# Performance work log

Hardware: AMD Instinct MI355X
Metric: run time of the kernel (lower is better)

## Reference

```python
import jax, jax.numpy as jnp
import numpy as np

EPS = 1e-5  # BatchNorm eps

def _bn(x):
    # BatchNorm1d(affine=False) in training mode: per-agent, per-feature batch stats
    m = jnp.mean(x, axis=1, keepdims=True)
    v = jnp.var(x, axis=1, keepdims=True)
    return (x - m) / jnp.sqrt(v + EPS)

def _lrelu(x):
    return jax.nn.leaky_relu(x, 0.01)

def setup_inputs() -> dict:
    key = jax.random.key(0)
    ks = jax.random.split(key, 14)
    A, B, IN, OUT, H, K = 8, 32768, 128, 32, 128, 4
    D = H // K
    s = 0.05
    return {
        "states": jax.random.normal(ks[0], (A, B, IN), jnp.float32),
        "actions": jax.random.normal(ks[1], (A, B, OUT), jnp.float32),
        "enc_w": jax.random.normal(ks[2], (A, IN + OUT, H), jnp.float32) * s,
        "enc_b": jax.random.normal(ks[3], (A, H), jnp.float32) * s,
        "aenc_w": jax.random.normal(ks[4], (A, OUT, H), jnp.float32) * s,
        "aenc_b": jax.random.normal(ks[5], (A, H), jnp.float32) * s,
        "key_w": jax.random.normal(ks[6], (K, H, D), jnp.float32) * s,
        "sel_w": jax.random.normal(ks[7], (K, H, D), jnp.float32) * s,
        "val_w": jax.random.normal(ks[8], (K, H, D), jnp.float32) * s,
        "val_b": jax.random.normal(ks[9], (K, D), jnp.float32) * s,
        "c1_w": jax.random.normal(ks[10], (A, 2 * H, H), jnp.float32) * s,
        "c1_b": jax.random.normal(ks[11], (A, H), jnp.float32) * s,
        "c2_w": jax.random.normal(ks[12], (A, H, 1), jnp.float32) * s,
        "c2_b": jax.random.normal(ks[13], (A, 1), jnp.float32) * s,
    }

def reference(states, actions, enc_w, enc_b, aenc_w, aenc_b,
              key_w, sel_w, val_w, val_b, c1_w, c1_b, c2_w, c2_b):
    A, B, _ = states.shape
    # per-agent state-action encodings: [A,B,H]
    sa = _bn(jnp.concatenate([states, actions], axis=-1))
    sa_enc = _lrelu(jnp.einsum('abi,aih->abh', sa, enc_w) + enc_b[:, None, :])
    # per-agent action encodings: [A,B,H]
    a_in = _bn(actions)
    a_enc = _lrelu(jnp.einsum('abi,aih->abh', a_in, aenc_w) + aenc_b[:, None, :])
    # per-head keys/values/selectors: [K,A,B,D]
    keys = jnp.einsum('abh,khd->kabd', a_enc, key_w)
    vals = _lrelu(jnp.einsum('abh,khd->kabd', a_enc, val_w) + val_b[:, None, None, :])
    sels = jnp.einsum('abh,khd->kabd', sa_enc, sel_w)
    D = keys.shape[-1]
    # attention logits over other agents: [K,B,A_query,A_key], self excluded
    logits = jnp.einsum('kibd,kjbd->kbij', sels, keys) / jnp.sqrt(jnp.float32(D))
    self_mask = jnp.eye(A, dtype=bool)[None, None]
    probs = jax.nn.softmax(jnp.where(self_mask, -jnp.inf, logits), axis=-1)
    # attended values: [K,A,B,D] -> concat heads -> [A,B,K*D]
    other = jnp.einsum('kbij,kjbd->kibd', probs, vals)
    other_cat = jnp.transpose(other, (1, 2, 0, 3)).reshape(A, B, -1)
    # per-agent critics on [sa_enc, attended]: [A,B,1]
    critic_in = jnp.concatenate([sa_enc, other_cat], axis=-1)
    h = _lrelu(jnp.einsum('abi,aih->abh', critic_in, c1_w) + c1_b[:, None, :])
    q = jnp.einsum('abh,aho->abo', h, c2_w) + c2_b[:, None, :]
    return q
```

## Files before the change

kernel.cpp:

```cpp
#include <hip/hip_runtime.h>
#include <hip/hip_bf16.h>
#include <stdint.h>

#define A_N 8
#define B_N 32768
#define IN_N 128
#define OUT_N 32
#define SAF 160
#define H_N 128
#define D_N 32
#define KD_N 128
#define CIN_N 256
#define CHUNKS 128
#define EPSV 1e-5f
#define ENC_KP 192

typedef unsigned int u32;
typedef unsigned short u16;
typedef __attribute__((ext_vector_type(8))) short short8;
typedef __attribute__((ext_vector_type(4))) float floatx4;

__device__ __forceinline__ float bf_lo(u32 u){ return __uint_as_float(u << 16); }
__device__ __forceinline__ float bf_hi(u32 u){ return __uint_as_float(u & 0xffff0000u); }
__device__ __forceinline__ float bf2f(u16 b){ return __uint_as_float(((u32)b) << 16); }
__device__ __forceinline__ u16 f2bf(float f){
  u32 u = __float_as_uint(f);
  return (u16)((u + 0x7fffu + ((u >> 16) & 1u)) >> 16);
}
__device__ __forceinline__ float lrelu(float x){ return x > 0.f ? x : 0.01f * x; }

__global__ __launch_bounds__(256) void k_stats(
    const float* __restrict__ states, const float* __restrict__ actions,
    float* __restrict__ part)
{
  int a = blockIdx.y;
  int chunk = blockIdx.x;
  int t = threadIdx.x;
  int r0 = chunk * (B_N / CHUNKS);
  __shared__ float red[512];
  {
    int f = t & 127, half = t >> 7;
    const float* p = states + ((size_t)a * B_N + r0 + half) * IN_N + f;
    float s1 = 0.f, s2 = 0.f;
    for (int it = 0; it < 128; ++it){
      float v = p[(size_t)(2 * it) * IN_N];
      s1 += v; s2 += v * v;
    }
    red[t] = s1; red[256 + t] = s2;
    __syncthreads();
    if (t < 128){
      float a1 = red[t] + red[t + 128];
      float a2 = red[256 + t] + red[256 + t + 128];
      size_t o = (((size_t)a * CHUNKS + chunk) * SAF + t) * 2;
      part[o] = a1; part[o + 1] = a2;
    }
    __syncthreads();
  }
  {
    int f = t & 31, g = t >> 5;
    const float* p = actions + ((size_t)a * B_N + r0 + g) * OUT_N + f;
    float s1 = 0.f, s2 = 0.f;
    for (int it = 0; it < 32; ++it){
      float v = p[(size_t)(8 * it) * OUT_N];
      s1 += v; s2 += v * v;
    }
    red[t] = s1; red[256 + t] = s2;
    __syncthreads();
    if (t < 32){
      float a1 = 0.f, a2 = 0.f;
      #pragma unroll
      for (int gg = 0; gg < 8; ++gg){
        a1 += red[t + 32 * gg];
        a2 += red[256 + t + 32 * gg];
      }
      size_t o = (((size_t)a * CHUNKS + chunk) * SAF + 128 + t) * 2;
      part[o] = a1; part[o + 1] = a2;
    }
  }
}

__global__ void k_finalize(const float* __restrict__ part,
                           float* __restrict__ meanArr, float* __restrict__ istdArr)
{
  int idx = blockIdx.x * blockDim.x + threadIdx.x;
  if (idx >= A_N * SAF) return;
  int a = idx / SAF, f = idx % SAF;
  float s1 = 0.f, s2 = 0.f;
  for (int c = 0; c < CHUNKS; ++c){
    size_t o = (((size_t)a * CHUNKS + c) * SAF + f) * 2;
    s1 += part[o]; s2 += part[o + 1];
  }
  float m = s1 * (1.f / B_N);
  float v = s2 * (1.f / B_N) - m * m;
  if (v < 0.f) v = 0.f;
  meanArr[idx] = m;
  istdArr[idx] = rsqrtf(v + EPSV);
}

__device__ __forceinline__ void packpair(float w, u16* __restrict__ dh,
                                         u16* __restrict__ dl, int i){
  u16 h = f2bf(w);
  dh[i] = h;
  dl[i] = f2bf(w - bf2f(h));
}

__global__ __launch_bounds__(256) void k_pack(
    const float* __restrict__ enc_w, const float* __restrict__ aenc_w,
    const float* __restrict__ key_w, const float* __restrict__ sel_w,
    const float* __restrict__ val_w, const float* __restrict__ c1_w,
    u16* __restrict__ encH, u16* __restrict__ encL,
    u16* __restrict__ aencH, u16* __restrict__ aencL,
    u16* __restrict__ keyH, u16* __restrict__ selH, u16* __restrict__ valH,
    u16* __restrict__ c1H, u16* __restrict__ c1L)
{
  int i = blockIdx.x * 256 + threadIdx.x;
  const int S0 = A_N * H_N * ENC_KP;
  const int S1 = A_N * H_N * OUT_N;
  const int S2 = KD_N * H_N;
  const int S5 = A_N * H_N * CIN_N;
  if (i < S0){
    int a = i / (H_N * ENC_KP); int r = i % (H_N * ENC_KP);
    int n = r / ENC_KP; int k = r % ENC_KP;
    float v = (k < SAF) ? enc_w[((size_t)a * SAF + k) * H_N + n] : 0.f;
    packpair(v, encH, encL, i);
    return;
  }
  i -= S0;
  if (i < S1){
    int a = i / (H_N * OUT_N); int r = i % (H_N * OUT_N);
    int n = r / OUT_N; int k = r % OUT_N;
    packpair(aenc_w[((size_t)a * OUT_N + k) * H_N + n], aencH, aencL, i);
    return;
  }
  i -= S1;
  if (i < 3 * S2){
    int which = i / S2; int j = i % S2;
    int n = j / H_N, k = j % H_N;
    const float* w = (which == 0) ? key_w : ((which == 1) ? sel_w : val_w);
    u16* dh = (which == 0) ? keyH : ((which == 1) ? selH : valH);
    dh[j] = f2bf(w[(((size_t)(n >> 5)) * H_N + k) * D_N + (n & 31)]);
    return;
  }
  i -= 3 * S2;
  if (i < S5){
    int a = i / (H_N * CIN_N); int r = i % (H_N * CIN_N);
    int n = r / CIN_N; int k = r % CIN_N;
    packpair(c1_w[((size_t)a * CIN_N + k) * H_N + n], c1H, c1L, i);
  }
}
#define PACK_TOTAL (A_N*H_N*ENC_KP + A_N*H_N*OUT_N + 3*KD_N*H_N + A_N*H_N*CIN_N)

__global__ __launch_bounds__(256, 3) void k_enc_sel(
    const float* __restrict__ states, const float* __restrict__ actions,
    const float* __restrict__ mean, const float* __restrict__ istd,
    const u16* __restrict__ encH, const u16* __restrict__ encL,
    const float* __restrict__ enc_b,
    const u16* __restrict__ selH,
    u16* __restrict__ sa_enc, u16* __restrict__ sels)
{
  int a = blockIdx.y; int row0 = blockIdx.x * 128; int t = threadIdx.x;
  int lane = t & 63, wave = t >> 6, l16 = lane & 15, quad = lane >> 4;
  __shared__ __align__(16) u16 S[22528];
  __shared__ __align__(16) float sc[192], sh[192];
  u16* Wh = S;
  u16* Wl = S + 5120;
  u16* Xh = S + 10240;
  u16* Xl = S + 15360;
  u16* T  = S;
  u16* Ws = S + 17408;

  if (t < 192){
    float m = 0.f, s = 0.f;
    if (t < SAF){ m = mean[a * SAF + t]; s = istd[a * SAF + t]; }
    sc[t] = s; sh[t] = -m * s;
  }
  floatx4 acc[2][8];
  #pragma unroll
  for (int mt = 0; mt < 2; ++mt)
    #pragma unroll
    for (int nt = 0; nt < 8; ++nt) acc[mt][nt] = (floatx4){0.f,0.f,0.f,0.f};
  const u16* wbh = encH + (size_t)a * H_N * ENC_KP;
  const u16* wbl = encL + (size_t)a * H_N * ENC_KP;
  __syncthreads();

  for (int k0 = 0; k0 < ENC_KP; k0 += 32){
    for (int c = t; c < 512; c += 256){
      int n = c >> 2, off = (c & 3) * 8;
      *(uint4*)&Wh[n * 40 + off] = *(const uint4*)(wbh + (size_t)n * ENC_KP + k0 + off);
      *(uint4*)&Wl[n * 40 + off] = *(const uint4*)(wbl + (size_t)n * ENC_KP + k0 + off);
    }
    for (int c = t; c < 1024; c += 256){
      int r = c >> 3, kc = (c & 7) * 4, f = k0 + kc;
      size_t row = (size_t)a * B_N + row0 + r;
      float4 v = {0.f, 0.f, 0.f, 0.f};
      if (f < IN_N)     v = *(const float4*)(states + row * IN_N + f);
      else if (f < SAF) v = *(const float4*)(actions + row * OUT_N + (f - IN_N));
      float4 scv = *(const float4*)&sc[f];
      float4 shv = *(const float4*)&sh[f];
      float x0 = fmaf(v.x, scv.x, shv.x), x1 = fmaf(v.y, scv.y, shv.y);
      float x2 = fmaf(v.z, scv.z, shv.z), x3 = fmaf(v.w, scv.w, shv.w);
      u16 h0 = f2bf(x0), h1 = f2bf(x1), h2 = f2bf(x2), h3 = f2bf(x3);
      *(u32*)&Xh[r * 40 + kc]     = (u32)h0 | ((u32)h1 << 16);
      *(u32*)&Xh[r * 40 + kc + 2] = (u32)h2 | ((u32)h3 << 16);
      u16 l0 = f2bf(x0 - bf2f(h0)), l1 = f2bf(x1 - bf2f(h1));
      u16 l2 = f2bf(x2 - bf2f(h2)), l3 = f2bf(x3 - bf2f(h3));
      *(u32*)&Xl[r * 40 + kc]     = (u32)l0 | ((u32)l1 << 16);
      *(u32*)&Xl[r * 40 + kc + 2] = (u32)l2 | ((u32)l3 << 16);
    }
    __syncthreads();
    {
      short8 ah[2], al[2], bh[8], bl[8];
      #pragma unroll
      for (int mt = 0; mt < 2; ++mt){
        int rr = (wave * 32 + mt * 16 + l16) * 40 + quad * 8;
        ah[mt] = *(const short8*)&Xh[rr];
        al[mt] = *(const short8*)&Xl[rr];
      }
      #pragma unroll
      for (int nt = 0; nt < 8; ++nt){
        int rr = (nt * 16 + l16) * 40 + quad * 8;
        bh[nt] = *(const short8*)&Wh[rr];
        bl[nt] = *(const short8*)&Wl[rr];
      }
      #pragma unroll
      for (int mt = 0; mt < 2; ++mt)
        #pragma unroll
        for (int nt = 0; nt < 8; ++nt){
          acc[mt][nt] = __builtin_amdgcn_mfma_f32_16x16x32_bf16(ah[mt], bh[nt], acc[mt][nt], 0,0,0);
          acc[mt][nt] = __builtin_amdgcn_mfma_f32_16x16x32_bf16(ah[mt], bl[nt], acc[mt][nt], 0,0,0);
          acc[mt][nt] = __builtin_amdgcn_mfma_f32_16x16x32_bf16(al[mt], bh[nt], acc[mt][nt], 0,0,0);
        }
    }
    __syncthreads();
  }

  {
    float bv[8];
    #pragma unroll
    for (int nt = 0; nt < 8; ++nt) bv[nt] = enc_b[a * H_N + nt * 16 + l16];
    #pragma unroll
    for (int mt = 0; mt < 2; ++mt)
      #pragma unroll
      for (int nt = 0; nt < 8; ++nt)
        #pragma unroll
        for (int r = 0; r < 4; ++r){
          int rl = wave * 32 + mt * 16 + quad * 4 + r;
          T[rl * 136 + nt * 16 + l16] = f2bf(lrelu(acc[mt][nt][r] + bv[nt]));
        }
  }
  __syncthreads();
  for (int c = t; c < 2048; c += 256){
    int row = c >> 4, col8 = (c & 15) * 8;
    *(uint4*)(sa_enc + ((size_t)a * B_N + row0 + row) * H_N + col8) =
        *(const uint4*)&T[row * 136 + col8];
  }

  #pragma unroll
  for (int mt = 0; mt < 2; ++mt)
    #pragma unroll
    for (int nt = 0; nt < 8; ++nt) acc[mt][nt] = (floatx4){0.f,0.f,0.f,0.f};
  for (int k0 = 0; k0 < H_N; k0 += 32){
    for (int c = t; c < 512; c += 256){
      int n = c >> 2, off = (c & 3) * 8;
      *(uint4*)&Ws[n * 40 + off] = *(const uint4*)(selH + (size_t)n * H_N + k0 + off);
    }
    __syncthreads();
    {
      short8 ah[2], bh[8];
      #pragma unroll
      for (int mt = 0; mt < 2; ++mt)
        ah[mt] = *(const short8*)&T[(wave * 32 + mt * 16 + l16) * 136 + k0 + quad * 8];
      #pragma unroll
      for (int nt = 0; nt < 8; ++nt)
        bh[nt] = *(const short8*)&Ws[(nt * 16 + l16) * 40 + quad * 8];
      #pragma unroll
      for (int mt = 0; mt < 2; ++mt)
        #pragma unroll
        for (int nt = 0; nt < 8; ++nt)
          acc[mt][nt] = __builtin_amdgcn_mfma_f32_16x16x32_bf16(ah[mt], bh[nt], acc[mt][nt], 0,0,0);
    }
    __syncthreads();
  }
  #pragma unroll
  for (int mt = 0; mt < 2; ++mt)
    #pragma unroll
    for (int nt = 0; nt < 8; ++nt)
      #pragma unroll
      for (int r = 0; r < 4; ++r){
        int rl = wave * 32 + mt * 16 + quad * 4 + r;
        T[rl * 136 + nt * 16 + l16] = f2bf(acc[mt][nt][r]);
      }
  __syncthreads();
  for (int c = t; c < 2048; c += 256){
    int row = c >> 4, col8 = (c & 15) * 8;
    *(uint4*)(sels + ((size_t)a * B_N + row0 + row) * H_N + col8) =
        *(const uint4*)&T[row * 136 + col8];
  }
}

__global__ __launch_bounds__(256, 2) void k_aenc_kv(
    const float* __restrict__ actions,
    const float* __restrict__ mean, const float* __restrict__ istd,
    const u16* __restrict__ aencH, const u16* __restrict__ aencL,
    const float* __restrict__ aenc_b,
    const u16* __restrict__ keyH, const u16* __restrict__ valH,
    const float* __restrict__ val_b,
    u16* __restrict__ keys, u16* __restrict__ vals)
{
  int a = blockIdx.y; int row0 = blockIdx.x * 128; int t = threadIdx.x;
  int lane = t & 63, wave = t >> 6, l16 = lane & 15, quad = lane >> 4;
  __shared__ __align__(16) u16 S[35840];
  __shared__ __align__(16) float sc[32], sh[32];
  u16* T  = S;
  u16* WK = S + 17408;
  u16* WV = S + 26624;
  u16* T2 = S + 17408;

  if (t < 32){
    float m = mean[a * SAF + 128 + t], s = istd[a * SAF + 128 + t];
    sc[t] = s; sh[t] = -m * s;
  }
  floatx4 accK[2][8], accV[2][8];
  #pragma unroll
  for (int mt = 0; mt < 2; ++mt)
    #pragma unroll
    for (int nt = 0; nt < 8; ++nt){
      accK[mt][nt] = (floatx4){0.f,0.f,0.f,0.f};
      accV[mt][nt] = (floatx4){0.f,0.f,0.f,0.f};
    }
  __syncthreads();

  {
    u16* Wh1 = S;  u16* Wl1 = S + 5120;
    u16* Xh = S + 10240; u16* Xl = S + 15360;
    const u16* wbh = aencH + (size_t)a * H_N * OUT_N;
    const u16* wbl = aencL + (size_t)a * H_N * OUT_N;
    for (int c = t; c < 512; c += 256){
      int n = c >> 2, off = (c & 3) * 8;
      *(uint4*)&Wh1[n * 40 + off] = *(const uint4*)(wbh + (size_t)n * OUT_N + off);
      *(uint4*)&Wl1[n * 40 + off] = *(const uint4*)(wbl + (size_t)n * OUT_N + off);
    }
    for (int c = t; c < 1024; c += 256){
      int r = c >> 3, kc = (c & 7) * 4;
      size_t row = (size_t)a * B_N + row0 + r;
      float4 v = *(const float4*)(actions + row * OUT_N + kc);
      float4 scv = *(const float4*)&sc[kc];
      float4 shv = *(const float4*)&sh[kc];
      float x0 = fmaf(v.x, scv.x, shv.x), x1 = fmaf(v.y, scv.y, shv.y);
      float x2 = fmaf(v.z, scv.z, shv.z), x3 = fmaf(v.w, scv.w, shv.w);
      u16 h0 = f2bf(x0), h1 = f2bf(x1), h2 = f2bf(x2), h3 = f2bf(x3);
      *(u32*)&Xh[r * 40 + kc]     = (u32)h0 | ((u32)h1 << 16);
      *(u32*)&Xh[r * 40 + kc + 2] = (u32)h2 | ((u32)h3 << 16);
      u16 l0 = f2bf(x0 - bf2f(h0)), l1 = f2bf(x1 - bf2f(h1));
      u16 l2 = f2bf(x2 - bf2f(h2)), l3 = f2bf(x3 - bf2f(h3));
      *(u32*)&Xl[r * 40 + kc]     = (u32)l0 | ((u32)l1 << 16);
      *(u32*)&Xl[r * 40 + kc + 2] = (u32)l2 | ((u32)l3 << 16);
    }
    __syncthreads();
    short8 ah[2], al[2], bh[8], bl[8];
    #pragma unroll
    for (int mt = 0; mt < 2; ++mt){
      int rr = (wave * 32 + mt * 16 + l16) * 40 + quad * 8;
      ah[mt] = *(const short8*)&Xh[rr];
      al[mt] = *(const short8*)&Xl[rr];
    }
    #pragma unroll
    for (int nt = 0; nt < 8; ++nt){
      int rr = (nt * 16 + l16) * 40 + quad * 8;
      bh[nt] = *(const short8*)&Wh1[rr];
      bl[nt] = *(const short8*)&Wl1[rr];
    }
    #pragma unroll
    for (int mt = 0; mt < 2; ++mt)
      #pragma unroll
      for (int nt = 0; nt < 8; ++nt){
        accK[mt][nt] = __builtin_amdgcn_mfma_f32_16x16x32_bf16(ah[mt], bh[nt], accK[mt][nt], 0,0,0);
        accK[mt][nt] = __builtin_amdgcn_mfma_f32_16x16x32_bf16(ah[mt], bl[nt], accK[mt][nt], 0,0,0);
        accK[mt][nt] = __builtin_amdgcn_mfma_f32_16x16x32_bf16(al[mt], bh[nt], accK[mt][nt], 0,0,0);
      }
    __syncthreads();
  }
  {
    float bv[8];
    #pragma unroll
    for (int nt = 0; nt < 8; ++nt) bv[nt] = aenc_b[a * H_N + nt * 16 + l16];
    #pragma unroll
    for (int mt = 0; mt < 2; ++mt)
      #pragma unroll
      for (int nt = 0; nt < 8; ++nt){
        #pragma unroll
        for (int r = 0; r < 4; ++r){
          int rl = wave * 32 + mt * 16 + quad * 4 + r;
          T[rl * 136 + nt * 16 + l16] = f2bf(lrelu(accK[mt][nt][r] + bv[nt]));
        }
        accK[mt][nt] = (floatx4){0.f,0.f,0.f,0.f};
      }
  }

  for (int k0 = 0; k0 < H_N; k0 += 64){
    __syncthreads();
    for (int c = t; c < 1024; c += 256){
      int n = c >> 3, off = (c & 7) * 8;
      *(uint4*)&WK[n * 72 + off] = *(const uint4*)(keyH + (size_t)n * H_N + k0 + off);
      *(uint4*)&WV[n * 72 + off] = *(const uint4*)(valH + (size_t)n * H_N + k0 + off);
    }
    __syncthreads();
    #pragma unroll
    for (int ks = 0; ks < 64; ks += 32){
      short8 ah[2], bk[8], bv[8];
      #pragma unroll
      for (int mt = 0; mt < 2; ++mt)
        ah[mt] = *(const short8*)&T[(wave * 32 + mt * 16 + l16) * 136 + k0 + ks + quad * 8];
      #pragma unroll
      for (int nt = 0; nt < 8; ++nt){
        int rr = (nt * 16 + l16) * 72 + ks + quad * 8;
        bk[nt] = *(const short8*)&WK[rr];
        bv[nt] = *(const short8*)&WV[rr];
      }
      #pragma unroll
      for (int mt = 0; mt < 2; ++mt)
        #pragma unroll
        for (int nt = 0; nt < 8; ++nt){
          accK[mt][nt] = __builtin_amdgcn_mfma_f32_16x16x32_bf16(ah[mt], bk[nt], accK[mt][nt], 0,0,0);
          accV[mt][nt] = __builtin_amdgcn_mfma_f32_16x16x32_bf16(ah[mt], bv[nt], accV[mt][nt], 0,0,0);
        }
    }
  }
  __syncthreads();
  {
    float bv[8];
    #pragma unroll
    for (int nt = 0; nt < 8; ++nt) bv[nt] = val_b[nt * 16 + l16];
    #pragma unroll
    for (int mt = 0; mt < 2; ++mt)
      #pragma unroll
      for (int nt = 0; nt < 8; ++nt)
        #pragma unroll
        for (int r = 0; r < 4; ++r){
          int rl = wave * 32 + mt * 16 + quad * 4 + r;
          T[rl * 136 + nt * 16 + l16]  = f2bf(lrelu(accV[mt][nt][r] + bv[nt]));
          T2[rl * 136 + nt * 16 + l16] = f2bf(accK[mt][nt][r]);
        }
  }
  __syncthreads();
  for (int c = t; c < 2048; c += 256){
    int row = c >> 4, col8 = (c & 15) * 8;
    *(uint4*)(vals + ((size_t)a * B_N + row0 + row) * H_N + col8) =
        *(const uint4*)&T[row * 136 + col8];
    *(uint4*)(keys + ((size_t)a * B_N + row0 + row) * H_N + col8) =
        *(const uint4*)&T2[row * 136 + col8];
  }
}

__global__ __launch_bounds__(256) void k_attn(
    const u16* __restrict__ sels, const u16* __restrict__ keys,
    const u16* __restrict__ vals, u16* __restrict__ other)
{
  int b0 = blockIdx.x * 8;
  int t = threadIdx.x;
  __shared__ __align__(16) u16 sS[8192], sK[8192], sV[8192];
  u32* dS = (u32*)sS; u32* dK = (u32*)sK; u32* dV = (u32*)sV;
  #pragma unroll
  for (int a = 0; a < 8; ++a){
    size_t go = ((size_t)a * B_N + b0) * KD_N;
    const u32* gs = (const u32*)(sels + go);
    const u32* gk = (const u32*)(keys + go);
    const u32* gv = (const u32*)(vals + go);
    dS[a * 512 + t] = gs[t]; dS[a * 512 + 256 + t] = gs[256 + t];
    dK[a * 512 + t] = gk[t]; dK[a * 512 + 256 + t] = gk[256 + t];
    dV[a * 512 + t] = gv[t]; dV[a * 512 + 256 + t] = gv[256 + t];
  }
  __syncthreads();
  int i = t & 7, p = t >> 3;
  int k = p & 3, bl = p >> 2;
  int base_i = (i * 8 + bl) * 128 + k * 32;
  float si[32];
  {
    const u32* S32 = (const u32*)&sS[base_i];
    #pragma unroll
    for (int d2 = 0; d2 < 16; ++d2){
      u32 u = S32[d2];
      si[2 * d2] = bf_lo(u); si[2 * d2 + 1] = bf_hi(u);
    }
  }
  float lg[8];
  #pragma unroll
  for (int j = 0; j < 8; ++j){
    const u32* K32 = (const u32*)&sK[(j * 8 + bl) * 128 + k * 32];
    float acc = 0.f;
    #pragma unroll
    for (int d2 = 0; d2 < 16; ++d2){
      u32 u = K32[d2];
      acc = fmaf(si[2 * d2], bf_lo(u), acc);
      acc = fmaf(si[2 * d2 + 1], bf_hi(u), acc);
    }
    lg[j] = acc * 0.17677669529663689f;
  }
  float mx = -3.0e38f;
  #pragma unroll
  for (int j = 0; j < 8; ++j) if (j != i) mx = fmaxf(mx, lg[j]);
  float pe[8], se = 0.f;
  #pragma unroll
  for (int j = 0; j < 8; ++j){
    pe[j] = (j == i) ? 0.f : __expf(lg[j] - mx);
    se += pe[j];
  }
  float inv = 1.f / se;
  #pragma unroll
  for (int j = 0; j < 8; ++j) pe[j] *= inv;
  __align__(16) u16 ob[32];
  #pragma unroll
  for (int d2 = 0; d2 < 16; ++d2){
    float acc0 = 0.f, acc1 = 0.f;
    #pragma unroll
    for (int j = 0; j < 8; ++j){
      u32 u = *(const u32*)&sV[(j * 8 + bl) * 128 + k * 32 + 2 * d2];
      acc0 = fmaf(pe[j], bf_lo(u), acc0);
      acc1 = fmaf(pe[j], bf_hi(u), acc1);
    }
    ob[2 * d2] = f2bf(acc0); ob[2 * d2 + 1] = f2bf(acc1);
  }
  uint4* dst = (uint4*)(other + ((size_t)i * B_N + (b0 + bl)) * KD_N + k * 32);
  const uint4* s4 = (const uint4*)ob;
  #pragma unroll
  for (int c = 0; c < 4; ++c) dst[c] = s4[c];
}

__global__ __launch_bounds__(256, 3) void k_critic(
    const u16* __restrict__ sa_enc, const u16* __restrict__ other,
    const u16* __restrict__ c1H, const u16* __restrict__ c1L,
    const float* __restrict__ c1_b,
    const float* __restrict__ c2w, const float* __restrict__ c2b,
    float* __restrict__ qout)
{
  int a = blockIdx.y; int row0 = blockIdx.x * 128; int t = threadIdx.x;
  int lane = t & 63, wave = t >> 6, l16 = lane & 15, quad = lane >> 4;
  __shared__ __align__(16) u16 Xs[5120];
  __shared__ __align__(16) u16 Wh[5120];
  __shared__ __align__(16) u16 Wl[5120];
  floatx4 acc[2][8];
  #pragma unroll
  for (int mt = 0; mt < 2; ++mt)
    #pragma unroll
    for (int nt = 0; nt < 8; ++nt) acc[mt][nt] = (floatx4){0.f,0.f,0.f,0.f};
  const u16* wbh = c1H + (size_t)a * H_N * CIN_N;
  const u16* wbl = c1L + (size_t)a * H_N * CIN_N;

  for (int k0 = 0; k0 < CIN_N; k0 += 32){
    for (int c = t; c < 512; c += 256){
      int n = c >> 2, off = (c & 3) * 8;
      *(uint4*)&Wh[n * 40 + off] = *(const uint4*)(wbh + (size_t)n * CIN_N + k0 + off);
      *(uint4*)&Wl[n * 40 + off] = *(const uint4*)(wbl + (size_t)n * CIN_N + k0 + off);
    }
    for (int c = t; c < 512; c += 256){
      int r = c >> 2, off = (c & 3) * 8;
      int fo = k0 + off;
      const u16* src = sa_enc;
      if (fo >= H_N){ src = other; fo -= H_N; }
      *(uint4*)&Xs[r * 40 + off] =
          *(const uint4*)(src + ((size_t)a * B_N + row0 + r) * H_N + fo);
    }
    __syncthreads();
    {
      short8 ah[2], bh[8], bl[8];
      #pragma unroll
      for (int mt = 0; mt < 2; ++mt)
        ah[mt] = *(const short8*)&Xs[(wave * 32 + mt * 16 + l16) * 40 + quad * 8];
      #pragma unroll
      for (int nt = 0; nt < 8; ++nt){
        int rr = (nt * 16 + l16) * 40 + quad * 8;
        bh[nt] = *(const short8*)&Wh[rr];
        bl[nt] = *(const short8*)&Wl[rr];
      }
      #pragma unroll
      for (int mt = 0; mt < 2; ++mt)
        #pragma unroll
        for (int nt = 0; nt < 8; ++nt){
          acc[mt][nt] = __builtin_amdgcn_mfma_f32_16x16x32_bf16(ah[mt], bh[nt], acc[mt][nt], 0,0,0);
          acc[mt][nt] = __builtin_amdgcn_mfma_f32_16x16x32_bf16(ah[mt], bl[nt], acc[mt][nt], 0,0,0);
        }
    }
    __syncthreads();
  }

  float c2r[8], bv[8];
  #pragma unroll
  for (int nt = 0; nt < 8; ++nt){
    c2r[nt] = c2w[a * H_N + nt * 16 + l16];
    bv[nt]  = c1_b[a * H_N + nt * 16 + l16];
  }
  #pragma unroll
  for (int mt = 0; mt < 2; ++mt){
    #pragma unroll
    for (int r = 0; r < 4; ++r){
      float s = 0.f;
      #pragma unroll
      for (int nt = 0; nt < 8; ++nt){
        float h = lrelu(acc[mt][nt][r] + bv[nt]);
        s = fmaf(h, c2r[nt], s);
      }
      s += __shfl_xor(s, 1);
      s += __shfl_xor(s, 2);
      s += __shfl_xor(s, 4);
      s += __shfl_xor(s, 8);
      if (l16 == 0){
        int row = row0 + wave * 32 + mt * 16 + quad * 4 + r;
        qout[(size_t)a * B_N + row] = s + c2b[a];
      }
    }
  }
}

extern "C" void kernel_launch(void* const* d_in, const int* in_sizes, int n_in,
                              void* d_out, int out_size, void* d_ws, size_t ws_size,
                              hipStream_t stream)
{
  const float* states  = (const float*)d_in[0];
  const float* actions = (const float*)d_in[1];
  const float* enc_w   = (const float*)d_in[2];
  const float* enc_b   = (const float*)d_in[3];
  const float* aenc_w  = (const float*)d_in[4];
  const float* aenc_b  = (const float*)d_in[5];
  const float* key_w   = (const float*)d_in[6];
  const float* sel_w   = (const float*)d_in[7];
  const float* val_w   = (const float*)d_in[8];
  const float* val_b   = (const float*)d_in[9];
  const float* c1_w    = (const float*)d_in[10];
  const float* c1_b    = (const float*)d_in[11];
  const float* c2_w    = (const float*)d_in[12];
  const float* c2_b    = (const float*)d_in[13];
  float* q = (float*)d_out;

  char* ws = (char*)d_ws;
  u16* encH  = (u16*)(ws + 0);
  u16* encL  = (u16*)(ws + 393216);
  u16* aencH = (u16*)(ws + 786432);
  u16* aencL = (u16*)(ws + 851968);
  u16* keyH  = (u16*)(ws + 917504);
  u16* selH  = (u16*)(ws + 950272);
  u16* valH  = (u16*)(ws + 983040);
  float* part    = (float*)ws;
  float* meanArr = (float*)(ws + 1310720);
  float* istdArr = (float*)(ws + 1315840);
  u16* c1H = (u16*)(ws + 1320960);
  u16* c1L = (u16*)(ws + 1845248);
  const size_t ibase = 4194304;
  const size_t BUF = (size_t)A_N * B_N * 128 * 2;
  u16* sa_enc = (u16*)(ws + ibase);
  u16* sels   = (u16*)(ws + ibase + BUF);
  u16* keys   = (u16*)(ws + ibase + 2 * BUF);
  u16* vals   = (u16*)(ws + ibase + 3 * BUF);

  k_stats<<<dim3(CHUNKS, A_N), 256, 0, stream>>>(states, actions, part);
  k_finalize<<<(A_N * SAF + 255) / 256, 256, 0, stream>>>(part, meanArr, istdArr);
  k_pack<<<(PACK_TOTAL + 255) / 256, 256, 0, stream>>>(
      enc_w, aenc_w, key_w, sel_w, val_w, c1_w,
      encH, encL, aencH, aencL, keyH, selH, valH, c1H, c1L);

  dim3 g(B_N / 128, A_N);
  k_enc_sel<<<g, 256, 0, stream>>>(states, actions, meanArr, istdArr,
                                   encH, encL, enc_b, selH, sa_enc, sels);
  k_aenc_kv<<<g, 256, 0, stream>>>(actions, meanArr, istdArr,
                                   aencH, aencL, aenc_b, keyH, valH, val_b,
                                   keys, vals);
  k_attn<<<B_N / 8, 256, 0, stream>>>(sels, keys, vals, keys);
  k_critic<<<g, 256, 0, stream>>>(sa_enc, keys, c1H, c1L, c1_b, c2_w, c2_b, q);
}
```

Baseline: 543.3 us.

## Load MFMA operands directly from global memory, drop LDS staging and c1 low-part split

The encoder, key/value and critic GEMMs now load A and B fragments straight from global memory into registers in MFMA layout, instead of staging tiles through LDS with barriers. LDS shrinks to a single output transpose buffer, and the keys/vals writeback reuses it in two passes. The critic weight is now packed as bf16 only, dropping the low-part correction and halving its MFMAs, which lowers precision. The enc_sel launch bound also drops from 3 to 2 waves per SIMD. Direct global fragment loads are less coalesced and rely on L2 caching of the weights.

```diff
diff --git a/kernel.cpp b/kernel.cpp
--- a/kernel.cpp
+++ b/kernel.cpp
@@ -111,7 +111,7 @@
     u16* __restrict__ encH, u16* __restrict__ encL,
     u16* __restrict__ aencH, u16* __restrict__ aencL,
     u16* __restrict__ keyH, u16* __restrict__ selH, u16* __restrict__ valH,
-    u16* __restrict__ c1H, u16* __restrict__ c1L)
+    u16* __restrict__ c1H)
 {
   int i = blockIdx.x * 256 + threadIdx.x;
   const int S0 = A_N * H_N * ENC_KP;
@@ -145,29 +145,22 @@
   if (i < S5){
     int a = i / (H_N * CIN_N); int r = i % (H_N * CIN_N);
     int n = r / CIN_N; int k = r % CIN_N;
-    packpair(c1_w[((size_t)a * CIN_N + k) * H_N + n], c1H, c1L, i);
+    c1H[i] = f2bf(c1_w[((size_t)a * CIN_N + k) * H_N + n]);
   }
 }
 #define PACK_TOTAL (A_N*H_N*ENC_KP + A_N*H_N*OUT_N + 3*KD_N*H_N + A_N*H_N*CIN_N)
 
-__global__ __launch_bounds__(256, 3) void k_enc_sel(
+__global__ __launch_bounds__(256, 2) void k_enc_sel(
     const float* __restrict__ states, const float* __restrict__ actions,
     const float* __restrict__ mean, const float* __restrict__ istd,
     const u16* __restrict__ encH, const u16* __restrict__ encL,
-    const float* __restrict__ enc_b,
-    const u16* __restrict__ selH,
+    const float* __restrict__ enc_b, const u16* __restrict__ selH,
     u16* __restrict__ sa_enc, u16* __restrict__ sels)
 {
   int a = blockIdx.y; int row0 = blockIdx.x * 128; int t = threadIdx.x;
   int lane = t & 63, wave = t >> 6, l16 = lane & 15, quad = lane >> 4;
-  __shared__ __align__(16) u16 S[22528];
+  __shared__ __align__(16) u16 T[128 * 136];
   __shared__ __align__(16) float sc[192], sh[192];
-  u16* Wh = S;
-  u16* Wl = S + 5120;
-  u16* Xh = S + 10240;
-  u16* Xl = S + 15360;
-  u16* T  = S;
-  u16* Ws = S + 17408;
 
   if (t < 192){
     float m = 0.f, s = 0.f;
@@ -183,55 +176,57 @@
   const u16* wbl = encL + (size_t)a * H_N * ENC_KP;
   __syncthreads();
 
-  for (int k0 = 0; k0 < ENC_KP; k0 += 32){
-    for (int c = t; c < 512; c += 256){
-      int n = c >> 2, off = (c & 3) * 8;
-      *(uint4*)&Wh[n * 40 + off] = *(const uint4*)(wbh + (size_t)n * ENC_KP + k0 + off);
-      *(uint4*)&Wl[n * 40 + off] = *(const uint4*)(wbl + (size_t)n * ENC_KP + k0 + off);
-    }
-    for (int c = t; c < 1024; c += 256){
-      int r = c >> 3, kc = (c & 7) * 4, f = k0 + kc;
-      size_t row = (size_t)a * B_N + row0 + r;
-      float4 v = {0.f, 0.f, 0.f, 0.f};
-      if (f < IN_N)     v = *(const float4*)(states + row * IN_N + f);
-      else if (f < SAF) v = *(const float4*)(actions + row * OUT_N + (f - IN_N));
-      float4 scv = *(const float4*)&sc[f];
-      float4 shv = *(const float4*)&sh[f];
-      float x0 = fmaf(v.x, scv.x, shv.x), x1 = fmaf(v.y, scv.y, shv.y);
-      float x2 = fmaf(v.z, scv.z, shv.z), x3 = fmaf(v.w, scv.w, shv.w);
-      u16 h0 = f2bf(x0), h1 = f2bf(x1), h2 = f2bf(x2), h3 = f2bf(x3);
-      *(u32*)&Xh[r * 40 + kc]     = (u32)h0 | ((u32)h1 << 16);
-      *(u32*)&Xh[r * 40 + kc + 2] = (u32)h2 | ((u32)h3 << 16);
-      u16 l0 = f2bf(x0 - bf2f(h0)), l1 = f2bf(x1 - bf2f(h1));
-      u16 l2 = f2bf(x2 - bf2f(h2)), l3 = f2bf(x3 - bf2f(h3));
-      *(u32*)&Xl[r * 40 + kc]     = (u32)l0 | ((u32)l1 << 16);
-      *(u32*)&Xl[r * 40 + kc + 2] = (u32)l2 | ((u32)l3 << 16);
-    }
-    __syncthreads();
-    {
-      short8 ah[2], al[2], bh[8], bl[8];
-      #pragma unroll
-      for (int mt = 0; mt < 2; ++mt){
-        int rr = (wave * 32 + mt * 16 + l16) * 40 + quad * 8;
-        ah[mt] = *(const short8*)&Xh[rr];
-        al[mt] = *(const short8*)&Xl[rr];
-      }
+  #pragma unroll
+  for (int kt = 0; kt < 5; ++kt){
+    int k0 = kt * 32;
+    int f0 = k0 + quad * 8;
+    float scv[8], shv[8];
+    *(float4*)&scv[0] = *(const float4*)&sc[f0];
+    *(float4*)&scv[4] = *(const float4*)&sc[f0 + 4];
+    *(float4*)&shv[0] = *(const float4*)&sh[f0];
+    *(float4*)&shv[4] = *(const float4*)&sh[f0 + 4];
+    short8 ah[2], al[2];
+    #pragma unroll
+    for (int mt = 0; mt < 2; ++mt){
+      size_t row = (size_t)a * B_N + row0 + wave * 32 + mt * 16 + l16;
+      float x[8];
+      if (kt < 4){
+        float4 v0 = *(const float4*)(states + row * IN_N + f0);
+        float4 v1 = *(const float4*)(states + row * IN_N + f0 + 4);
+        x[0]=v0.x; x[1]=v0.y; x[2]=v0.z; x[3]=v0.w;
+        x[4]=v1.x; x[5]=v1.y; x[6]=v1.z; x[7]=v1.w;
+      } else {
+        int fo = f0 - IN_N;
+        float4 v0 = *(const float4*)(actions + row * OUT_N + fo);
+        float4 v1 = *(const float4*)(actions + row * OUT_N + fo + 4);
+        x[0]=v0.x; x[1]=v0.y; x[2]=v0.z; x[3]=v0.w;
+        x[4]=v1.x; x[5]=v1.y; x[6]=v1.z; x[7]=v1.w;
+      }
+      short8 hv, lv;
+      #pragma unroll
+      for (int e = 0; e < 8; ++e){
+        float xx = fmaf(x[e], scv[e], shv[e]);
+        u16 hb = f2bf(xx);
+        hv[e] = (short)hb;
+        lv[e] = (short)f2bf(xx - bf2f(hb));
+      }
+      ah[mt] = hv; al[mt] = lv;
+    }
+    short8 bh[8], bl[8];
+    #pragma unroll
+    for (int nt = 0; nt < 8; ++nt){
+      size_t wo = (size_t)(nt * 16 + l16) * ENC_KP + f0;
+      bh[nt] = *(const short8*)(wbh + wo);
+      bl[nt] = *(const short8*)(wbl + wo);
+    }
+    #pragma unroll
+    for (int mt = 0; mt < 2; ++mt)
       #pragma unroll
       for (int nt = 0; nt < 8; ++nt){
-        int rr = (nt * 16 + l16) * 40 + quad * 8;
-        bh[nt] = *(const short8*)&Wh[rr];
-        bl[nt] = *(const short8*)&Wl[rr];
-      }
-      #pragma unroll
-      for (int mt = 0; mt < 2; ++mt)
-        #pragma unroll
-        for (int nt = 0; nt < 8; ++nt){
-          acc[mt][nt] = __builtin_amdgcn_mfma_f32_16x16x32_bf16(ah[mt], bh[nt], acc[mt][nt], 0,0,0);
-          acc[mt][nt] = __builtin_amdgcn_mfma_f32_16x16x32_bf16(ah[mt], bl[nt], acc[mt][nt], 0,0,0);
-          acc[mt][nt] = __builtin_amdgcn_mfma_f32_16x16x32_bf16(al[mt], bh[nt], acc[mt][nt], 0,0,0);
-        }
-    }
-    __syncthreads();
+        acc[mt][nt] = __builtin_amdgcn_mfma_f32_16x16x32_bf16(ah[mt], bh[nt], acc[mt][nt], 0,0,0);
+        acc[mt][nt] = __builtin_amdgcn_mfma_f32_16x16x32_bf16(ah[mt], bl[nt], acc[mt][nt], 0,0,0);
+        acc[mt][nt] = __builtin_amdgcn_mfma_f32_16x16x32_bf16(al[mt], bh[nt], acc[mt][nt], 0,0,0);
+      }
   }
 
   {
@@ -259,28 +254,23 @@
   for (int mt = 0; mt < 2; ++mt)
     #pragma unroll
     for (int nt = 0; nt < 8; ++nt) acc[mt][nt] = (floatx4){0.f,0.f,0.f,0.f};
-  for (int k0 = 0; k0 < H_N; k0 += 32){
-    for (int c = t; c < 512; c += 256){
-      int n = c >> 2, off = (c & 3) * 8;
-      *(uint4*)&Ws[n * 40 + off] = *(const uint4*)(selH + (size_t)n * H_N + k0 + off);
-    }
-    __syncthreads();
-    {
-      short8 ah[2], bh[8];
-      #pragma unroll
-      for (int mt = 0; mt < 2; ++mt)
-        ah[mt] = *(const short8*)&T[(wave * 32 + mt * 16 + l16) * 136 + k0 + quad * 8];
+  #pragma unroll
+  for (int kt = 0; kt < 4; ++kt){
+    int f0 = kt * 32 + quad * 8;
+    short8 aT[2], bw[8];
+    #pragma unroll
+    for (int mt = 0; mt < 2; ++mt)
+      aT[mt] = *(const short8*)&T[(wave * 32 + mt * 16 + l16) * 136 + f0];
+    #pragma unroll
+    for (int nt = 0; nt < 8; ++nt)
+      bw[nt] = *(const short8*)(selH + (size_t)(nt * 16 + l16) * H_N + f0);
+    #pragma unroll
+    for (int mt = 0; mt < 2; ++mt)
       #pragma unroll
       for (int nt = 0; nt < 8; ++nt)
-        bh[nt] = *(const short8*)&Ws[(nt * 16 + l16) * 40 + quad * 8];
-      #pragma unroll
-      for (int mt = 0; mt < 2; ++mt)
-        #pragma unroll
-        for (int nt = 0; nt < 8; ++nt)
-          acc[mt][nt] = __builtin_amdgcn_mfma_f32_16x16x32_bf16(ah[mt], bh[nt], acc[mt][nt], 0,0,0);
-    }
-    __syncthreads();
-  }
+        acc[mt][nt] = __builtin_amdgcn_mfma_f32_16x16x32_bf16(aT[mt], bw[nt], acc[mt][nt], 0,0,0);
+  }
+  __syncthreads();
   #pragma unroll
   for (int mt = 0; mt < 2; ++mt)
     #pragma unroll
@@ -309,12 +299,8 @@
 {
   int a = blockIdx.y; int row0 = blockIdx.x * 128; int t = threadIdx.x;
   int lane = t & 63, wave = t >> 6, l16 = lane & 15, quad = lane >> 4;
-  __shared__ __align__(16) u16 S[35840];
+  __shared__ __align__(16) u16 T[128 * 136];
   __shared__ __align__(16) float sc[32], sh[32];
-  u16* T  = S;
-  u16* WK = S + 17408;
-  u16* WV = S + 26624;
-  u16* T2 = S + 17408;
 
   if (t < 32){
     float m = mean[a * SAF + 128 + t], s = istd[a * SAF + 128 + t];
@@ -328,47 +314,40 @@
       accK[mt][nt] = (floatx4){0.f,0.f,0.f,0.f};
       accV[mt][nt] = (floatx4){0.f,0.f,0.f,0.f};
     }
+  const u16* wbh = aencH + (size_t)a * H_N * OUT_N;
+  const u16* wbl = aencL + (size_t)a * H_N * OUT_N;
   __syncthreads();
 
   {
-    u16* Wh1 = S;  u16* Wl1 = S + 5120;
-    u16* Xh = S + 10240; u16* Xl = S + 15360;
-    const u16* wbh = aencH + (size_t)a * H_N * OUT_N;
-    const u16* wbl = aencL + (size_t)a * H_N * OUT_N;
-    for (int c = t; c < 512; c += 256){
-      int n = c >> 2, off = (c & 3) * 8;
-      *(uint4*)&Wh1[n * 40 + off] = *(const uint4*)(wbh + (size_t)n * OUT_N + off);
-      *(uint4*)&Wl1[n * 40 + off] = *(const uint4*)(wbl + (size_t)n * OUT_N + off);
-    }
-    for (int c = t; c < 1024; c += 256){
-      int r = c >> 3, kc = (c & 7) * 4;
-      size_t row = (size_t)a * B_N + row0 + r;
-      float4 v = *(const float4*)(actions + row * OUT_N + kc);
-      float4 scv = *(const float4*)&sc[kc];
-      float4 shv = *(const float4*)&sh[kc];
-      float x0 = fmaf(v.x, scv.x, shv.x), x1 = fmaf(v.y, scv.y, shv.y);
-      float x2 = fmaf(v.z, scv.z, shv.z), x3 = fmaf(v.w, scv.w, shv.w);
-      u16 h0 = f2bf(x0), h1 = f2bf(x1), h2 = f2bf(x2), h3 = f2bf(x3);
-      *(u32*)&Xh[r * 40 + kc]     = (u32)h0 | ((u32)h1 << 16);
-      *(u32*)&Xh[r * 40 + kc + 2] = (u32)h2 | ((u32)h3 << 16);
-      u16 l0 = f2bf(x0 - bf2f(h0)), l1 = f2bf(x1 - bf2f(h1));
-      u16 l2 = f2bf(x2 - bf2f(h2)), l3 = f2bf(x3 - bf2f(h3));
-      *(u32*)&Xl[r * 40 + kc]     = (u32)l0 | ((u32)l1 << 16);
-      *(u32*)&Xl[r * 40 + kc + 2] = (u32)l2 | ((u32)l3 << 16);
-    }
-    __syncthreads();
-    short8 ah[2], al[2], bh[8], bl[8];
+    int f0 = quad * 8;
+    float scv[8], shv[8];
+    *(float4*)&scv[0] = *(const float4*)&sc[f0];
+    *(float4*)&scv[4] = *(const float4*)&sc[f0 + 4];
+    *(float4*)&shv[0] = *(const float4*)&sh[f0];
+    *(float4*)&shv[4] = *(const float4*)&sh[f0 + 4];
+    short8 ah[2], al[2];
     #pragma unroll
     for (int mt = 0; mt < 2; ++mt){
-      int rr = (wave * 32 + mt * 16 + l16) * 40 + quad * 8;
-      ah[mt] = *(const short8*)&Xh[rr];
-      al[mt] = *(const short8*)&Xl[rr];
-    }
+      size_t row = (size_t)a * B_N + row0 + wave * 32 + mt * 16 + l16;
+      float4 v0 = *(const float4*)(actions + row * OUT_N + f0);
+      float4 v1 = *(const float4*)(actions + row * OUT_N + f0 + 4);
+      float x[8] = {v0.x, v0.y, v0.z, v0.w, v1.x, v1.y, v1.z, v1.w};
+      short8 hv, lv;
+      #pragma unroll
+      for (int e = 0; e < 8; ++e){
+        float xx = fmaf(x[e], scv[e], shv[e]);
+        u16 hb = f2bf(xx);
+        hv[e] = (short)hb;
+        lv[e] = (short)f2bf(xx - bf2f(hb));
+      }
+      ah[mt] = hv; al[mt] = lv;
+    }
+    short8 bh[8], bl[8];
     #pragma unroll
     for (int nt = 0; nt < 8; ++nt){
-      int rr = (nt * 16 + l16) * 40 + quad * 8;
-      bh[nt] = *(const short8*)&Wh1[rr];
-      bl[nt] = *(const short8*)&Wl1[rr];
+      size_t wo = (size_t)(nt * 16 + l16) * OUT_N + f0;
+      bh[nt] = *(const short8*)(wbh + wo);
+      bl[nt] = *(const short8*)(wbl + wo);
     }
     #pragma unroll
     for (int mt = 0; mt < 2; ++mt)
@@ -378,7 +357,6 @@
         accK[mt][nt] = __builtin_amdgcn_mfma_f32_16x16x32_bf16(ah[mt], bl[nt], accK[mt][nt], 0,0,0);
         accK[mt][nt] = __builtin_amdgcn_mfma_f32_16x16x32_bf16(al[mt], bh[nt], accK[mt][nt], 0,0,0);
       }
-    __syncthreads();
   }
   {
     float bv[8];
@@ -396,37 +374,31 @@
         accK[mt][nt] = (floatx4){0.f,0.f,0.f,0.f};
       }
   }
-
-  for (int k0 = 0; k0 < H_N; k0 += 64){
-    __syncthreads();
-    for (int c = t; c < 1024; c += 256){
-      int n = c >> 3, off = (c & 7) * 8;
-      *(uint4*)&WK[n * 72 + off] = *(const uint4*)(keyH + (size_t)n * H_N + k0 + off);
-      *(uint4*)&WV[n * 72 + off] = *(const uint4*)(valH + (size_t)n * H_N + k0 + off);
-    }
-    __syncthreads();
-    #pragma unroll
-    for (int ks = 0; ks < 64; ks += 32){
-      short8 ah[2], bk[8], bv[8];
-      #pragma unroll
-      for (int mt = 0; mt < 2; ++mt)
-        ah[mt] = *(const short8*)&T[(wave * 32 + mt * 16 + l16) * 136 + k0 + ks + quad * 8];
+  __syncthreads();
+
+  #pragma unroll
+  for (int kt = 0; kt < 4; ++kt){
+    int f0 = kt * 32 + quad * 8;
+    short8 aT[2], bk[8], bv2[8];
+    #pragma unroll
+    for (int mt = 0; mt < 2; ++mt)
+      aT[mt] = *(const short8*)&T[(wave * 32 + mt * 16 + l16) * 136 + f0];
+    #pragma unroll
+    for (int nt = 0; nt < 8; ++nt){
+      size_t wo = (size_t)(nt * 16 + l16) * H_N + f0;
+      bk[nt]  = *(const short8*)(keyH + wo);
+      bv2[nt] = *(const short8*)(valH + wo);
+    }
+    #pragma unroll
+    for (int mt = 0; mt < 2; ++mt)
       #pragma unroll
       for (int nt = 0; nt < 8; ++nt){
-        int rr = (nt * 16 + l16) * 72 + ks + quad * 8;
-        bk[nt] = *(const short8*)&WK[rr];
-        bv[nt] = *(const short8*)&WV[rr];
-      }
-      #pragma unroll
-      for (int mt = 0; mt < 2; ++mt)
-        #pragma unroll
-        for (int nt = 0; nt < 8; ++nt){
-          accK[mt][nt] = __builtin_amdgcn_mfma_f32_16x16x32_bf16(ah[mt], bk[nt], accK[mt][nt], 0,0,0);
-          accV[mt][nt] = __builtin_amdgcn_mfma_f32_16x16x32_bf16(ah[mt], bv[nt], accV[mt][nt], 0,0,0);
-        }
-    }
-  }
-  __syncthreads();
+        accK[mt][nt] = __builtin_amdgcn_mfma_f32_16x16x32_bf16(aT[mt], bk[nt],  accK[mt][nt], 0,0,0);
+        accV[mt][nt] = __builtin_amdgcn_mfma_f32_16x16x32_bf16(aT[mt], bv2[nt], accV[mt][nt], 0,0,0);
+      }
+  }
+  __syncthreads();
+
   {
     float bv[8];
     #pragma unroll
@@ -438,8 +410,7 @@
         #pragma unroll
         for (int r = 0; r < 4; ++r){
           int rl = wave * 32 + mt * 16 + quad * 4 + r;
-          T[rl * 136 + nt * 16 + l16]  = f2bf(lrelu(accV[mt][nt][r] + bv[nt]));
-          T2[rl * 136 + nt * 16 + l16] = f2bf(accK[mt][nt][r]);
+          T[rl * 136 + nt * 16 + l16] = f2bf(lrelu(accV[mt][nt][r] + bv[nt]));
         }
   }
   __syncthreads();
@@ -447,8 +418,22 @@
     int row = c >> 4, col8 = (c & 15) * 8;
     *(uint4*)(vals + ((size_t)a * B_N + row0 + row) * H_N + col8) =
         *(const uint4*)&T[row * 136 + col8];
+  }
+  __syncthreads();
+  #pragma unroll
+  for (int mt = 0; mt < 2; ++mt)
+    #pragma unroll
+    for (int nt = 0; nt < 8; ++nt)
+      #pragma unroll
+      for (int r = 0; r < 4; ++r){
+        int rl = wave * 32 + mt * 16 + quad * 4 + r;
+        T[rl * 136 + nt * 16 + l16] = f2bf(accK[mt][nt][r]);
+      }
+  __syncthreads();
+  for (int c = t; c < 2048; c += 256){
+    int row = c >> 4, col8 = (c & 15) * 8;
     *(uint4*)(keys + ((size_t)a * B_N + row0 + row) * H_N + col8) =
-        *(const uint4*)&T2[row * 136 + col8];
+        *(const uint4*)&T[row * 136 + col8];
   }
 }
 
@@ -528,59 +513,40 @@
 
 __global__ __launch_bounds__(256, 3) void k_critic(
     const u16* __restrict__ sa_enc, const u16* __restrict__ other,
-    const u16* __restrict__ c1H, const u16* __restrict__ c1L,
-    const float* __restrict__ c1_b,
+    const u16* __restrict__ c1H, const float* __restrict__ c1_b,
     const float* __restrict__ c2w, const float* __restrict__ c2b,
     float* __restrict__ qout)
 {
   int a = blockIdx.y; int row0 = blockIdx.x * 128; int t = threadIdx.x;
   int lane = t & 63, wave = t >> 6, l16 = lane & 15, quad = lane >> 4;
-  __shared__ __align__(16) u16 Xs[5120];
-  __shared__ __align__(16) u16 Wh[5120];
-  __shared__ __align__(16) u16 Wl[5120];
   floatx4 acc[2][8];
   #pragma unroll
   for (int mt = 0; mt < 2; ++mt)
     #pragma unroll
     for (int nt = 0; nt < 8; ++nt) acc[mt][nt] = (floatx4){0.f,0.f,0.f,0.f};
-  const u16* wbh = c1H + (size_t)a * H_N * CIN_N;
-  const u16* wbl = c1L + (size_t)a * H_N * CIN_N;
-
-  for (int k0 = 0; k0 < CIN_N; k0 += 32){
-    for (int c = t; c < 512; c += 256){
-      int n = c >> 2, off = (c & 3) * 8;
-      *(uint4*)&Wh[n * 40 + off] = *(const uint4*)(wbh + (size_t)n * CIN_N + k0 + off);
-      *(uint4*)&Wl[n * 40 + off] = *(const uint4*)(wbl + (size_t)n * CIN_N + k0 + off);
-    }
-    for (int c = t; c < 512; c += 256){
-      int r = c >> 2, off = (c & 3) * 8;
-      int fo = k0 + off;
-      const u16* src = sa_enc;
-      if (fo >= H_N){ src = other; fo -= H_N; }
-      *(uint4*)&Xs[r * 40 + off] =
-          *(const uint4*)(src + ((size_t)a * B_N + row0 + r) * H_N + fo);
-    }
-    __syncthreads();
-    {
-      short8 ah[2], bh[8], bl[8];
-      #pragma unroll
-      for (int mt = 0; mt < 2; ++mt)
-        ah[mt] = *(const short8*)&Xs[(wave * 32 + mt * 16 + l16) * 40 + quad * 8];
-      #pragma unroll
-      for (int nt = 0; nt < 8; ++nt){
-        int rr = (nt * 16 + l16) * 40 + quad * 8;
-        bh[nt] = *(const short8*)&Wh[rr];
-        bl[nt] = *(const short8*)&Wl[rr];
-      }
-      #pragma unroll
-      for (int mt = 0; mt < 2; ++mt)
-        #pragma unroll
-        for (int nt = 0; nt < 8; ++nt){
-          acc[mt][nt] = __builtin_amdgcn_mfma_f32_16x16x32_bf16(ah[mt], bh[nt], acc[mt][nt], 0,0,0);
-          acc[mt][nt] = __builtin_amdgcn_mfma_f32_16x16x32_bf16(ah[mt], bl[nt], acc[mt][nt], 0,0,0);
-        }
-    }
-    __syncthreads();
+  const u16* wb = c1H + (size_t)a * H_N * CIN_N;
+  size_t rbase[2];
+  #pragma unroll
+  for (int mt = 0; mt < 2; ++mt)
+    rbase[mt] = ((size_t)a * B_N + row0 + wave * 32 + mt * 16 + l16) * H_N;
+
+  #pragma unroll
+  for (int kt = 0; kt < 8; ++kt){
+    int k0 = kt * 32;
+    int fo = (k0 & 127) + quad * 8;
+    const u16* src = (kt < 4) ? sa_enc : other;
+    short8 ah[2], bh[8];
+    #pragma unroll
+    for (int mt = 0; mt < 2; ++mt)
+      ah[mt] = *(const short8*)(src + rbase[mt] + fo);
+    #pragma unroll
+    for (int nt = 0; nt < 8; ++nt)
+      bh[nt] = *(const short8*)(wb + (size_t)(nt * 16 + l16) * CIN_N + k0 + quad * 8);
+    #pragma unroll
+    for (int mt = 0; mt < 2; ++mt)
+      #pragma unroll
+      for (int nt = 0; nt < 8; ++nt)
+        acc[mt][nt] = __builtin_amdgcn_mfma_f32_16x16x32_bf16(ah[mt], bh[nt], acc[mt][nt], 0,0,0);
   }
 
   float c2r[8], bv[8];
@@ -643,7 +609,6 @@
   float* meanArr = (float*)(ws + 1310720);
   float* istdArr = (float*)(ws + 1315840);
   u16* c1H = (u16*)(ws + 1320960);
-  u16* c1L = (u16*)(ws + 1845248);
   const size_t ibase = 4194304;
   const size_t BUF = (size_t)A_N * B_N * 128 * 2;
   u16* sa_enc = (u16*)(ws + ibase);
@@ -655,7 +620,7 @@
   k_finalize<<<(A_N * SAF + 255) / 256, 256, 0, stream>>>(part, meanArr, istdArr);
   k_pack<<<(PACK_TOTAL + 255) / 256, 256, 0, stream>>>(
       enc_w, aenc_w, key_w, sel_w, val_w, c1_w,
-      encH, encL, aencH, aencL, keyH, selH, valH, c1H, c1L);
+      encH, encL, aencH, aencL, keyH, selH, valH, c1H);
 
   dim3 g(B_N / 128, A_N);
   k_enc_sel<<<g, 256, 0, stream>>>(states, actions, meanArr, istdArr,
@@ -664,5 +629,5 @@
                                    aencH, aencL, aenc_b, keyH, valH, val_b,
                                    keys, vals);
   k_attn<<<B_N / 8, 256, 0, stream>>>(sels, keys, vals, keys);
-  k_critic<<<g, 256, 0, stream>>>(sa_enc, keys, c1H, c1L, c1_b, c2_w, c2_b, q);
-}
+  k_critic<<<g, 256, 0, stream>>>(sa_enc, keys, c1H, c1_b, c2_w, c2_b, q);
+}
```

After: 636.9 us. +17.2%, slower.
